# Performance work log

Measured on AMD Instinct MI355X. Metric: run time of the kernel, lower is better.

## Reference

```python
import jax, jax.numpy as jnp
import numpy as np

B, T, H, I, O = 256, 8192, 16, 1, 1


def setup_inputs() -> dict:
    key = jax.random.key(0)
    ks = jax.random.split(key, 8)
    s = 1.0 / np.sqrt(H)  # PyTorch default init scale
    x = jax.random.normal(ks[0], (B, T, I), dtype=jnp.float32)
    h0 = jax.random.normal(ks[1], (1, B, H), dtype=jnp.float32)
    W_ih = jax.random.uniform(ks[2], (H, I), jnp.float32, -s, s)
    W_hh = jax.random.uniform(ks[3], (H, H), jnp.float32, -s, s)
    b_ih = jax.random.uniform(ks[4], (H,), jnp.float32, -s, s)
    b_hh = jax.random.uniform(ks[5], (H,), jnp.float32, -s, s)
    W_out = jax.random.uniform(ks[6], (O, H), jnp.float32, -s, s)
    b_out = jax.random.uniform(ks[7], (O,), jnp.float32, -s, s)
    return {"x": x, "h0": h0, "W_ih": W_ih, "W_hh": W_hh,
            "b_ih": b_ih, "b_hh": b_hh, "W_out": W_out, "b_out": b_out}


def reference(x, h0, W_ih, W_hh, b_ih, b_hh, W_out, b_out):
    # Precompute input projection for all timesteps: [T, B, H]
    xp = jnp.einsum('bti,hi->tbh', x, W_ih) + b_ih + b_hh

    def step(h, xt):
        h_new = jnp.tanh(xt + h @ W_hh.T)  # [B, H]
        return h_new, h_new

    hT, outs = jax.lax.scan(step, h0[0], xp)  # hT: [B,H], outs: [T,B,H]
    out_flat = outs.transpose(1, 0, 2).reshape(-1, H)  # [B*T, H]
    out = (out_flat @ W_out.T + b_out)[None]  # [1, B*T, O]
    return out, hT[None]  # hidden: [1, B, H]
```

## Files before the change

### kernel.cpp

```cpp
#include <hip/hip_runtime.h>

#define ROTI(v, CTRL) __builtin_amdgcn_update_dpp(0, (v), (CTRL), 0xF, 0xF, true)

constexpr int T_LEN  = 8192;
constexpr int BATCH  = 256;
constexpr int HID    = 16;
constexpr int RING   = 128;
constexpr int SLOT_W = 68;
constexpr int CHUNK  = 32;

#define MATVEC(a0_, a1_, a2_, a3_, h_)                                                  \
  asm("s_nop 1\n\t"                                                                     \
      "v_fmac_f32 %[a0], %[h], %[w0]\n\t"                                               \
      "v_mul_f32_dpp %[a1], %[h], %[w4] row_ror:4 row_mask:0xf bank_mask:0xf\n\t"       \
      "v_mul_f32_dpp %[a2], %[h], %[w8] row_ror:8 row_mask:0xf bank_mask:0xf\n\t"       \
      "v_mul_f32_dpp %[a3], %[h], %[w12] row_ror:12 row_mask:0xf bank_mask:0xf\n\t"     \
      "v_fmac_f32_dpp %[a0], %[h], %[w1] row_ror:1 row_mask:0xf bank_mask:0xf\n\t"      \
      "v_fmac_f32_dpp %[a1], %[h], %[w5] row_ror:5 row_mask:0xf bank_mask:0xf\n\t"      \
      "v_fmac_f32_dpp %[a2], %[h], %[w9] row_ror:9 row_mask:0xf bank_mask:0xf\n\t"      \
      "v_fmac_f32_dpp %[a3], %[h], %[w13] row_ror:13 row_mask:0xf bank_mask:0xf\n\t"    \
      "v_fmac_f32_dpp %[a0], %[h], %[w2] row_ror:2 row_mask:0xf bank_mask:0xf\n\t"      \
      "v_fmac_f32_dpp %[a1], %[h], %[w6] row_ror:6 row_mask:0xf bank_mask:0xf\n\t"      \
      "v_fmac_f32_dpp %[a2], %[h], %[w10] row_ror:10 row_mask:0xf bank_mask:0xf\n\t"    \
      "v_fmac_f32_dpp %[a3], %[h], %[w14] row_ror:14 row_mask:0xf bank_mask:0xf\n\t"    \
      "v_fmac_f32_dpp %[a0], %[h], %[w3] row_ror:3 row_mask:0xf bank_mask:0xf\n\t"      \
      "v_fmac_f32_dpp %[a1], %[h], %[w7] row_ror:7 row_mask:0xf bank_mask:0xf\n\t"      \
      "v_fmac_f32_dpp %[a2], %[h], %[w11] row_ror:11 row_mask:0xf bank_mask:0xf\n\t"    \
      "v_fmac_f32_dpp %[a3], %[h], %[w15] row_ror:15 row_mask:0xf bank_mask:0xf\n\t"    \
      : [a0]"+v"(a0_), [a1]"=&v"(a1_), [a2]"=&v"(a2_), [a3]"=&v"(a3_)                  \
      : [h]"v"(h_),                                                                     \
        [w0]"v"(wr0),  [w1]"v"(wr1),  [w2]"v"(wr2),  [w3]"v"(wr3),                      \
        [w4]"v"(wr4),  [w5]"v"(wr5),  [w6]"v"(wr6),  [w7]"v"(wr7),                      \
        [w8]"v"(wr8),  [w9]"v"(wr9),  [w10]"v"(wr10), [w11]"v"(wr11),                   \
        [w12]"v"(wr12), [w13]"v"(wr13), [w14]"v"(wr14), [w15]"v"(wr15))

#define STEP(XV) do {                                                                   \
    float a0 = fmaf((XV), wihK, biasK), a1, a2, a3;                                     \
    MATVEC(a0, a1, a2, a3, h);                                                          \
    float s = (a0 + a1) + (a2 + a3);                                                    \
    float e = __builtin_amdgcn_exp2f(s);                                                \
    h = fmaf(-2.0f, __builtin_amdgcn_rcpf(e + 1.0f), 1.0f);                             \
    *rp = h; rp += SLOT_W;                                                              \
} while (0)

#define BLOCK16(C0, C1, C2, C3) do {                                                    \
    STEP(C0.x); STEP(C0.y); STEP(C0.z); STEP(C0.w);                                     \
    STEP(C1.x); STEP(C1.y); STEP(C1.z); STEP(C1.w);                                     \
    STEP(C2.x); STEP(C2.y); STEP(C2.z); STEP(C2.w);                                     \
    STEP(C3.x); STEP(C3.y); STEP(C3.z); STEP(C3.w);                                     \
} while (0)

__global__ void __launch_bounds__(128, 1)
rnn_fused(const float* __restrict__ x,
          const float* __restrict__ hinit,
          const float* __restrict__ Wih,
          const float* __restrict__ Whh,
          const float* __restrict__ bih,
          const float* __restrict__ bhh,
          const float* __restrict__ Wout,
          const float* __restrict__ boutp,
          float* __restrict__ out)
{
    __shared__ float ring[RING * SLOT_W];
    __shared__ int   syncc[2];
    volatile int* prodc = &syncc[0];
    volatile int* consc = &syncc[1];

    const int tid = (int)threadIdx.x;
    if (tid == 0) { syncc[0] = 0; syncc[1] = 0; }
    __syncthreads();

    if (tid < 64) {
        const int j = tid & 15;
        const int g = tid >> 4;
        const int b = (int)blockIdx.x * 4 + g;

        const int pr  = ROTI(j, 0x121);
        const int dir = (__builtin_amdgcn_readfirstlane(pr) == 1) ? 1 : -1;

        const float K2 = 2.8853900817779268f;
        float wr0  = K2 * Whh[j * HID + ((j + dir * 0)  & 15)];
        float wr1  = K2 * Whh[j * HID + ((j + dir * 1)  & 15)];
        float wr2  = K2 * Whh[j * HID + ((j + dir * 2)  & 15)];
        float wr3  = K2 * Whh[j * HID + ((j + dir * 3)  & 15)];
        float wr4  = K2 * Whh[j * HID + ((j + dir * 4)  & 15)];
        float wr5  = K2 * Whh[j * HID + ((j + dir * 5)  & 15)];
        float wr6  = K2 * Whh[j * HID + ((j + dir * 6)  & 15)];
        float wr7  = K2 * Whh[j * HID + ((j + dir * 7)  & 15)];
        float wr8  = K2 * Whh[j * HID + ((j + dir * 8)  & 15)];
        float wr9  = K2 * Whh[j * HID + ((j + dir * 9)  & 15)];
        float wr10 = K2 * Whh[j * HID + ((j + dir * 10) & 15)];
        float wr11 = K2 * Whh[j * HID + ((j + dir * 11) & 15)];
        float wr12 = K2 * Whh[j * HID + ((j + dir * 12) & 15)];
        float wr13 = K2 * Whh[j * HID + ((j + dir * 13) & 15)];
        float wr14 = K2 * Whh[j * HID + ((j + dir * 14) & 15)];
        float wr15 = K2 * Whh[j * HID + ((j + dir * 15) & 15)];

        const float wihK  = K2 * Wih[j];
        const float biasK = K2 * (bih[j] + bhh[j]);

        float h = hinit[b * HID + j];
        const float* xb = x + (size_t)b * T_LEN;

        float4 c0 = ((const float4*)xb)[0], c1 = ((const float4*)xb)[1],
               c2 = ((const float4*)xb)[2], c3 = ((const float4*)xb)[3];

        for (int t0 = 0; t0 < T_LEN; t0 += 16) {
            if ((t0 & (CHUNK - 1)) == 0) {
                const int need = t0 + CHUNK - RING;
                if (need > 0) {
                    while (*consc < need) { }
                    __asm__ volatile("" ::: "memory");
                }
            }
            const int tn = (t0 + 16) & (T_LEN - 1);
            const float* q = xb + tn;
            float4 n0 = ((const float4*)q)[0], n1 = ((const float4*)q)[1],
                   n2 = ((const float4*)q)[2], n3 = ((const float4*)q)[3];

            float* rp = &ring[(t0 & (RING - 1)) * SLOT_W + g * 17 + j];
            BLOCK16(c0, c1, c2, c3);
            c0 = n0; c1 = n1; c2 = n2; c3 = n3;

            if (((t0 + 16) & (CHUNK - 1)) == 0) {
                __asm__ volatile("s_waitcnt lgkmcnt(0)" ::: "memory");
                *prodc = t0 + 16;
            }
        }

        out[(size_t)BATCH * T_LEN + (size_t)b * HID + j] = h;
    } else {
        const int lane = tid - 64;
        const int tt   = lane & 15;
        const int bs   = lane >> 4;
        const int bg   = (int)blockIdx.x * 4 + bs;

        const float w0  = Wout[0],  w1  = Wout[1],  w2  = Wout[2],  w3  = Wout[3];
        const float w4  = Wout[4],  w5  = Wout[5],  w6  = Wout[6],  w7  = Wout[7];
        const float w8  = Wout[8],  w9  = Wout[9],  w10 = Wout[10], w11 = Wout[11];
        const float w12 = Wout[12], w13 = Wout[13], w14 = Wout[14], w15 = Wout[15];
        const float bo  = boutp[0];

        float* ob = out + (size_t)bg * T_LEN;

        for (int t0 = 0; t0 < T_LEN; t0 += 16) {
            while (*prodc < t0 + 16) { }
            __asm__ volatile("" ::: "memory");

            const float* hr = &ring[((t0 + tt) & (RING - 1)) * SLOT_W + bs * 17];
            float o = bo;
            o = fmaf(hr[0],  w0,  o);
            o = fmaf(hr[1],  w1,  o);
            o = fmaf(hr[2],  w2,  o);
            o = fmaf(hr[3],  w3,  o);
            o = fmaf(hr[4],  w4,  o);
            o = fmaf(hr[5],  w5,  o);
            o = fmaf(hr[6],  w6,  o);
            o = fmaf(hr[7],  w7,  o);
            o = fmaf(hr[8],  w8,  o);
            o = fmaf(hr[9],  w9,  o);
            o = fmaf(hr[10], w10, o);
            o = fmaf(hr[11], w11, o);
            o = fmaf(hr[12], w12, o);
            o = fmaf(hr[13], w13, o);
            o = fmaf(hr[14], w14, o);
            o = fmaf(hr[15], w15, o);
            ob[t0 + tt] = o;

            *consc = t0 + 16;
        }
    }
}

extern "C" void kernel_launch(void* const* d_in, const int* in_sizes, int n_in,
                              void* d_out, int out_size, void* d_ws, size_t ws_size,
                              hipStream_t stream)
{
    const float* x    = (const float*)d_in[0];
    const float* h0   = (const float*)d_in[1];
    const float* Wih  = (const float*)d_in[2];
    const float* Whh  = (const float*)d_in[3];
    const float* bih  = (const float*)d_in[4];
    const float* bhh  = (const float*)d_in[5];
    const float* Wout = (const float*)d_in[6];
    const float* bout = (const float*)d_in[7];
    float* out = (float*)d_out;

    rnn_fused<<<dim3(BATCH / 4), dim3(128), 0, stream>>>(
        x, h0, Wih, Whh, bih, bhh, Wout, bout, out);
}
```

Measured before the change: 541.7 us.

## Interleave two batch recurrences per wavefront and halve the grid

Each producer wavefront now advances two independent batch chains (A and B) together. A single inline-asm block interleaves their DPP matvec with two accumulators each, followed by the exp/rcp tanh, so one chain's instruction latency can be hidden behind the other's. The grid drops from 64 to 32 blocks. The shared ring changes to 64 slots of width 129, and the producer/consumer handshake now happens every 16 steps instead of every 32. The trade-off: each wave issues roughly twice as many instructions per timestep, while the number of sequential timesteps is unchanged.

After: 993.0 us. 83.3% more time.

```diff
diff --git a/kernel.cpp b/kernel.cpp
--- a/kernel.cpp
+++ b/kernel.cpp
@@ -5,49 +5,67 @@
 constexpr int T_LEN  = 8192;
 constexpr int BATCH  = 256;
 constexpr int HID    = 16;
-constexpr int RING   = 128;
-constexpr int SLOT_W = 68;
-constexpr int CHUNK  = 32;
-
-#define MATVEC(a0_, a1_, a2_, a3_, h_)                                                  \
-  asm("s_nop 1\n\t"                                                                     \
-      "v_fmac_f32 %[a0], %[h], %[w0]\n\t"                                               \
-      "v_mul_f32_dpp %[a1], %[h], %[w4] row_ror:4 row_mask:0xf bank_mask:0xf\n\t"       \
-      "v_mul_f32_dpp %[a2], %[h], %[w8] row_ror:8 row_mask:0xf bank_mask:0xf\n\t"       \
-      "v_mul_f32_dpp %[a3], %[h], %[w12] row_ror:12 row_mask:0xf bank_mask:0xf\n\t"     \
-      "v_fmac_f32_dpp %[a0], %[h], %[w1] row_ror:1 row_mask:0xf bank_mask:0xf\n\t"      \
-      "v_fmac_f32_dpp %[a1], %[h], %[w5] row_ror:5 row_mask:0xf bank_mask:0xf\n\t"      \
-      "v_fmac_f32_dpp %[a2], %[h], %[w9] row_ror:9 row_mask:0xf bank_mask:0xf\n\t"      \
-      "v_fmac_f32_dpp %[a3], %[h], %[w13] row_ror:13 row_mask:0xf bank_mask:0xf\n\t"    \
-      "v_fmac_f32_dpp %[a0], %[h], %[w2] row_ror:2 row_mask:0xf bank_mask:0xf\n\t"      \
-      "v_fmac_f32_dpp %[a1], %[h], %[w6] row_ror:6 row_mask:0xf bank_mask:0xf\n\t"      \
-      "v_fmac_f32_dpp %[a2], %[h], %[w10] row_ror:10 row_mask:0xf bank_mask:0xf\n\t"    \
-      "v_fmac_f32_dpp %[a3], %[h], %[w14] row_ror:14 row_mask:0xf bank_mask:0xf\n\t"    \
-      "v_fmac_f32_dpp %[a0], %[h], %[w3] row_ror:3 row_mask:0xf bank_mask:0xf\n\t"      \
-      "v_fmac_f32_dpp %[a1], %[h], %[w7] row_ror:7 row_mask:0xf bank_mask:0xf\n\t"      \
-      "v_fmac_f32_dpp %[a2], %[h], %[w11] row_ror:11 row_mask:0xf bank_mask:0xf\n\t"    \
-      "v_fmac_f32_dpp %[a3], %[h], %[w15] row_ror:15 row_mask:0xf bank_mask:0xf\n\t"    \
-      : [a0]"+v"(a0_), [a1]"=&v"(a1_), [a2]"=&v"(a2_), [a3]"=&v"(a3_)                  \
-      : [h]"v"(h_),                                                                     \
-        [w0]"v"(wr0),  [w1]"v"(wr1),  [w2]"v"(wr2),  [w3]"v"(wr3),                      \
-        [w4]"v"(wr4),  [w5]"v"(wr5),  [w6]"v"(wr6),  [w7]"v"(wr7),                      \
-        [w8]"v"(wr8),  [w9]"v"(wr9),  [w10]"v"(wr10), [w11]"v"(wr11),                   \
+constexpr int RING   = 64;
+constexpr int SLOT_W = 129;
+
+#define STEP2(aA0_, aB0_, hA_, hB_)                                                    \
+  asm("s_nop 1\n\t"                                                                    \
+      "v_fmac_f32 %[aA0], %[hA], %[w0]\n\t"                                            \
+      "v_fmac_f32 %[aB0], %[hB], %[w0]\n\t"                                            \
+      "v_mul_f32_dpp %[aA1], %[hA], %[w1] row_ror:1 row_mask:0xf bank_mask:0xf\n\t"    \
+      "v_mul_f32_dpp %[aB1], %[hB], %[w1] row_ror:1 row_mask:0xf bank_mask:0xf\n\t"    \
+      "v_fmac_f32_dpp %[aA0], %[hA], %[w2] row_ror:2 row_mask:0xf bank_mask:0xf\n\t"   \
+      "v_fmac_f32_dpp %[aB0], %[hB], %[w2] row_ror:2 row_mask:0xf bank_mask:0xf\n\t"   \
+      "v_fmac_f32_dpp %[aA1], %[hA], %[w3] row_ror:3 row_mask:0xf bank_mask:0xf\n\t"   \
+      "v_fmac_f32_dpp %[aB1], %[hB], %[w3] row_ror:3 row_mask:0xf bank_mask:0xf\n\t"   \
+      "v_fmac_f32_dpp %[aA0], %[hA], %[w4] row_ror:4 row_mask:0xf bank_mask:0xf\n\t"   \
+      "v_fmac_f32_dpp %[aB0], %[hB], %[w4] row_ror:4 row_mask:0xf bank_mask:0xf\n\t"   \
+      "v_fmac_f32_dpp %[aA1], %[hA], %[w5] row_ror:5 row_mask:0xf bank_mask:0xf\n\t"   \
+      "v_fmac_f32_dpp %[aB1], %[hB], %[w5] row_ror:5 row_mask:0xf bank_mask:0xf\n\t"   \
+      "v_fmac_f32_dpp %[aA0], %[hA], %[w6] row_ror:6 row_mask:0xf bank_mask:0xf\n\t"   \
+      "v_fmac_f32_dpp %[aB0], %[hB], %[w6] row_ror:6 row_mask:0xf bank_mask:0xf\n\t"   \
+      "v_fmac_f32_dpp %[aA1], %[hA], %[w7] row_ror:7 row_mask:0xf bank_mask:0xf\n\t"   \
+      "v_fmac_f32_dpp %[aB1], %[hB], %[w7] row_ror:7 row_mask:0xf bank_mask:0xf\n\t"   \
+      "v_fmac_f32_dpp %[aA0], %[hA], %[w8] row_ror:8 row_mask:0xf bank_mask:0xf\n\t"   \
+      "v_fmac_f32_dpp %[aB0], %[hB], %[w8] row_ror:8 row_mask:0xf bank_mask:0xf\n\t"   \
+      "v_fmac_f32_dpp %[aA1], %[hA], %[w9] row_ror:9 row_mask:0xf bank_mask:0xf\n\t"   \
+      "v_fmac_f32_dpp %[aB1], %[hB], %[w9] row_ror:9 row_mask:0xf bank_mask:0xf\n\t"   \
+      "v_fmac_f32_dpp %[aA0], %[hA], %[w10] row_ror:10 row_mask:0xf bank_mask:0xf\n\t" \
+      "v_fmac_f32_dpp %[aB0], %[hB], %[w10] row_ror:10 row_mask:0xf bank_mask:0xf\n\t" \
+      "v_fmac_f32_dpp %[aA1], %[hA], %[w11] row_ror:11 row_mask:0xf bank_mask:0xf\n\t" \
+      "v_fmac_f32_dpp %[aB1], %[hB], %[w11] row_ror:11 row_mask:0xf bank_mask:0xf\n\t" \
+      "v_fmac_f32_dpp %[aA0], %[hA], %[w12] row_ror:12 row_mask:0xf bank_mask:0xf\n\t" \
+      "v_fmac_f32_dpp %[aB0], %[hB], %[w12] row_ror:12 row_mask:0xf bank_mask:0xf\n\t" \
+      "v_fmac_f32_dpp %[aA1], %[hA], %[w13] row_ror:13 row_mask:0xf bank_mask:0xf\n\t" \
+      "v_fmac_f32_dpp %[aB1], %[hB], %[w13] row_ror:13 row_mask:0xf bank_mask:0xf\n\t" \
+      "v_fmac_f32_dpp %[aA0], %[hA], %[w14] row_ror:14 row_mask:0xf bank_mask:0xf\n\t" \
+      "v_fmac_f32_dpp %[aB0], %[hB], %[w14] row_ror:14 row_mask:0xf bank_mask:0xf\n\t" \
+      "v_fmac_f32_dpp %[aA1], %[hA], %[w15] row_ror:15 row_mask:0xf bank_mask:0xf\n\t" \
+      "v_fmac_f32_dpp %[aB1], %[hB], %[w15] row_ror:15 row_mask:0xf bank_mask:0xf\n\t" \
+      "v_add_f32 %[aA0], %[aA0], %[aA1]\n\t"                                           \
+      "v_add_f32 %[aB0], %[aB0], %[aB1]\n\t"                                           \
+      "v_exp_f32 %[aA1], %[aA0]\n\t"                                                   \
+      "v_exp_f32 %[aB1], %[aB0]\n\t"                                                   \
+      "v_add_f32 %[aA0], 1.0, %[aA1]\n\t"                                              \
+      "v_add_f32 %[aB0], 1.0, %[aB1]\n\t"                                              \
+      "v_rcp_f32 %[aA1], %[aA0]\n\t"                                                   \
+      "v_rcp_f32 %[aB1], %[aB0]\n\t"                                                   \
+      "v_fma_f32 %[hA], -2.0, %[aA1], 1.0\n\t"                                         \
+      "v_fma_f32 %[hB], -2.0, %[aB1], 1.0\n\t"                                         \
+      : [aA0]"+v"(aA0_), [aB0]"+v"(aB0_),                                              \
+        [aA1]"=&v"(tmpA), [aB1]"=&v"(tmpB),                                            \
+        [hA]"+v"(hA_), [hB]"+v"(hB_)                                                   \
+      : [w0]"v"(wr0),  [w1]"v"(wr1),  [w2]"v"(wr2),  [w3]"v"(wr3),                     \
+        [w4]"v"(wr4),  [w5]"v"(wr5),  [w6]"v"(wr6),  [w7]"v"(wr7),                     \
+        [w8]"v"(wr8),  [w9]"v"(wr9),  [w10]"v"(wr10), [w11]"v"(wr11),                  \
         [w12]"v"(wr12), [w13]"v"(wr13), [w14]"v"(wr14), [w15]"v"(wr15))
 
-#define STEP(XV) do {                                                                   \
-    float a0 = fmaf((XV), wihK, biasK), a1, a2, a3;                                     \
-    MATVEC(a0, a1, a2, a3, h);                                                          \
-    float s = (a0 + a1) + (a2 + a3);                                                    \
-    float e = __builtin_amdgcn_exp2f(s);                                                \
-    h = fmaf(-2.0f, __builtin_amdgcn_rcpf(e + 1.0f), 1.0f);                             \
-    *rp = h; rp += SLOT_W;                                                              \
-} while (0)
-
-#define BLOCK16(C0, C1, C2, C3) do {                                                    \
-    STEP(C0.x); STEP(C0.y); STEP(C0.z); STEP(C0.w);                                     \
-    STEP(C1.x); STEP(C1.y); STEP(C1.z); STEP(C1.w);                                     \
-    STEP(C2.x); STEP(C2.y); STEP(C2.z); STEP(C2.w);                                     \
-    STEP(C3.x); STEP(C3.y); STEP(C3.z); STEP(C3.w);                                     \
+#define POSITION(XA, XB, POS) do {                                                     \
+    float aA0 = fmaf((XA), wihK, biasK);                                               \
+    float aB0 = fmaf((XB), wihK, biasK);                                               \
+    STEP2(aA0, aB0, hA, hB);                                                           \
+    rp[(POS) * SLOT_W]      = hA;                                                      \
+    rp[(POS) * SLOT_W + 64] = hB;                                                      \
 } while (0)
 
 __global__ void __launch_bounds__(128, 1)
@@ -73,7 +91,8 @@
     if (tid < 64) {
         const int j = tid & 15;
         const int g = tid >> 4;
-        const int b = (int)blockIdx.x * 4 + g;
+        const int bA = (int)blockIdx.x * 8 + g;
+        const int bB = bA + 4;
 
         const int pr  = ROTI(j, 0x121);
         const int dir = (__builtin_amdgcn_readfirstlane(pr) == 1) ? 1 : -1;
@@ -99,41 +118,66 @@
         const float wihK  = K2 * Wih[j];
         const float biasK = K2 * (bih[j] + bhh[j]);
 
-        float h = hinit[b * HID + j];
-        const float* xb = x + (size_t)b * T_LEN;
-
-        float4 c0 = ((const float4*)xb)[0], c1 = ((const float4*)xb)[1],
-               c2 = ((const float4*)xb)[2], c3 = ((const float4*)xb)[3];
+        float hA = hinit[bA * HID + j];
+        float hB = hinit[bB * HID + j];
+        float tmpA, tmpB;
+
+        const float* xbA = x + (size_t)bA * T_LEN;
+        const float* xbB = x + (size_t)bB * T_LEN;
+
+        float4 qA0 = ((const float4*)xbA)[0], qA1 = ((const float4*)xbA)[1],
+               qA2 = ((const float4*)xbA)[2], qA3 = ((const float4*)xbA)[3];
+        float4 qB0 = ((const float4*)xbB)[0], qB1 = ((const float4*)xbB)[1],
+               qB2 = ((const float4*)xbB)[2], qB3 = ((const float4*)xbB)[3];
 
         for (int t0 = 0; t0 < T_LEN; t0 += 16) {
-            if ((t0 & (CHUNK - 1)) == 0) {
-                const int need = t0 + CHUNK - RING;
-                if (need > 0) {
-                    while (*consc < need) { }
-                    __asm__ volatile("" ::: "memory");
-                }
+            const int need = t0 + 16 - RING;
+            if (need > 0) {
+                while (*consc < need) { }
+                __asm__ volatile("" ::: "memory");
             }
             const int tn = (t0 + 16) & (T_LEN - 1);
-            const float* q = xb + tn;
-            float4 n0 = ((const float4*)q)[0], n1 = ((const float4*)q)[1],
-                   n2 = ((const float4*)q)[2], n3 = ((const float4*)q)[3];
-
-            float* rp = &ring[(t0 & (RING - 1)) * SLOT_W + g * 17 + j];
-            BLOCK16(c0, c1, c2, c3);
-            c0 = n0; c1 = n1; c2 = n2; c3 = n3;
-
-            if (((t0 + 16) & (CHUNK - 1)) == 0) {
-                __asm__ volatile("s_waitcnt lgkmcnt(0)" ::: "memory");
-                *prodc = t0 + 16;
-            }
+            const float* qa = xbA + tn;
+            const float* qb = xbB + tn;
+            float4 nA0 = ((const float4*)qa)[0], nA1 = ((const float4*)qa)[1],
+                   nA2 = ((const float4*)qa)[2], nA3 = ((const float4*)qa)[3];
+            float4 nB0 = ((const float4*)qb)[0], nB1 = ((const float4*)qb)[1],
+                   nB2 = ((const float4*)qb)[2], nB3 = ((const float4*)qb)[3];
+
+            float* rp = &ring[(t0 & (RING - 1)) * SLOT_W + g * 16 + j];
+
+            POSITION(qA0.x, qB0.x, 0);
+            POSITION(qA0.y, qB0.y, 1);
+            POSITION(qA0.z, qB0.z, 2);
+            POSITION(qA0.w, qB0.w, 3);
+            POSITION(qA1.x, qB1.x, 4);
+            POSITION(qA1.y, qB1.y, 5);
+            POSITION(qA1.z, qB1.z, 6);
+            POSITION(qA1.w, qB1.w, 7);
+            POSITION(qA2.x, qB2.x, 8);
+            POSITION(qA2.y, qB2.y, 9);
+            POSITION(qA2.z, qB2.z, 10);
+            POSITION(qA2.w, qB2.w, 11);
+            POSITION(qA3.x, qB3.x, 12);
+            POSITION(qA3.y, qB3.y, 13);
+            POSITION(qA3.z, qB3.z, 14);
+            POSITION(qA3.w, qB3.w, 15);
+
+            qA0 = nA0; qA1 = nA1; qA2 = nA2; qA3 = nA3;
+            qB0 = nB0; qB1 = nB1; qB2 = nB2; qB3 = nB3;
+
+            __asm__ volatile("s_waitcnt lgkmcnt(0)" ::: "memory");
+            *prodc = t0 + 16;
         }
 
-        out[(size_t)BATCH * T_LEN + (size_t)b * HID + j] = h;
+        out[(size_t)BATCH * T_LEN + (size_t)bA * HID + j] = hA;
+        out[(size_t)BATCH * T_LEN + (size_t)bB * HID + j] = hB;
     } else {
         const int lane = tid - 64;
         const int tt   = lane & 15;
         const int bs   = lane >> 4;
-        const int bg   = (int)blockIdx.x * 4 + bs;
+        const int bgA  = (int)blockIdx.x * 8 + bs;
+        const int bgB  = bgA + 4;
 
         const float w0  = Wout[0],  w1  = Wout[1],  w2  = Wout[2],  w3  = Wout[3];
         const float w4  = Wout[4],  w5  = Wout[5],  w6  = Wout[6],  w7  = Wout[7];
@@ -141,31 +185,40 @@
         const float w12 = Wout[12], w13 = Wout[13], w14 = Wout[14], w15 = Wout[15];
         const float bo  = boutp[0];
 
-        float* ob = out + (size_t)bg * T_LEN;
+        float* obA = out + (size_t)bgA * T_LEN;
+        float* obB = out + (size_t)bgB * T_LEN;
 
         for (int t0 = 0; t0 < T_LEN; t0 += 16) {
             while (*prodc < t0 + 16) { }
             __asm__ volatile("" ::: "memory");
 
-            const float* hr = &ring[((t0 + tt) & (RING - 1)) * SLOT_W + bs * 17];
-            float o = bo;
-            o = fmaf(hr[0],  w0,  o);
-            o = fmaf(hr[1],  w1,  o);
-            o = fmaf(hr[2],  w2,  o);
-            o = fmaf(hr[3],  w3,  o);
-            o = fmaf(hr[4],  w4,  o);
-            o = fmaf(hr[5],  w5,  o);
-            o = fmaf(hr[6],  w6,  o);
-            o = fmaf(hr[7],  w7,  o);
-            o = fmaf(hr[8],  w8,  o);
-            o = fmaf(hr[9],  w9,  o);
-            o = fmaf(hr[10], w10, o);
-            o = fmaf(hr[11], w11, o);
-            o = fmaf(hr[12], w12, o);
-            o = fmaf(hr[13], w13, o);
-            o = fmaf(hr[14], w14, o);
-            o = fmaf(hr[15], w15, o);
-            ob[t0 + tt] = o;
+            const float* base = &ring[((t0 + tt) & (RING - 1)) * SLOT_W + bs * 16];
+            {
+                const float* hr = base;
+                float o = bo;
+                o = fmaf(hr[0],  w0,  o); o = fmaf(hr[1],  w1,  o);
+                o = fmaf(hr[2],  w2,  o); o = fmaf(hr[3],  w3,  o);
+                o = fmaf(hr[4],  w4,  o); o = fmaf(hr[5],  w5,  o);
+                o = fmaf(hr[6],  w6,  o); o = fmaf(hr[7],  w7,  o);
+                o = fmaf(hr[8],  w8,  o); o = fmaf(hr[9],  w9,  o);
+                o = fmaf(hr[10], w10, o); o = fmaf(hr[11], w11, o);
+                o = fmaf(hr[12], w12, o); o = fmaf(hr[13], w13, o);
+                o = fmaf(hr[14], w14, o); o = fmaf(hr[15], w15, o);
+                obA[t0 + tt] = o;
+            }
+            {
+                const float* hr = base + 64;
+                float o = bo;
+                o = fmaf(hr[0],  w0,  o); o = fmaf(hr[1],  w1,  o);
+                o = fmaf(hr[2],  w2,  o); o = fmaf(hr[3],  w3,  o);
+                o = fmaf(hr[4],  w4,  o); o = fmaf(hr[5],  w5,  o);
+                o = fmaf(hr[6],  w6,  o); o = fmaf(hr[7],  w7,  o);
+                o = fmaf(hr[8],  w8,  o); o = fmaf(hr[9],  w9,  o);
+                o = fmaf(hr[10], w10, o); o = fmaf(hr[11], w11, o);
+                o = fmaf(hr[12], w12, o); o = fmaf(hr[13], w13, o);
+                o = fmaf(hr[14], w14, o); o = fmaf(hr[15], w15, o);
+                obB[t0 + tt] = o;
+            }
 
             *consc = t0 + 16;
         }
@@ -186,6 +239,6 @@
     const float* bout = (const float*)d_in[7];
     float* out = (float*)d_out;
 
-    rnn_fused<<<dim3(BATCH / 4), dim3(128), 0, stream>>>(
+    rnn_fused<<<dim3(BATCH / 8), dim3(128), 0, stream>>>(
         x, h0, Wih, Whh, bih, bhh, Wout, bout, out);
 }
```

## Use packed fp16 dot products for recurrence and output projection

Applied to the files above, without the earlier changes.

Packs the hidden state and recurrent weights into fp16 pairs, using v_dot2 with DPP-shuffled operands to halve the multiply-add count per step. The rcp instruction is replaced with a bit-trick initial guess plus two Newton steps. The ring buffer stores packed halves, shrinks, and is synchronized every 16 steps. This trades accuracy (fp16 hidden state and weights across a long recurrence) and extra DPP and convert latency on the serial chain for fewer FMAs.

New measurement: 592.3 us. 9.3% more time.

```diff
diff --git a/kernel.cpp b/kernel.cpp
--- a/kernel.cpp
+++ b/kernel.cpp
@@ -1,53 +1,44 @@
 #include <hip/hip_runtime.h>
 
-#define ROTI(v, CTRL) __builtin_amdgcn_update_dpp(0, (v), (CTRL), 0xF, 0xF, true)
+typedef decltype(__builtin_amdgcn_cvt_pkrtz(0.0f, 0.0f)) h2;
+
+#define DPPI(v, CTRL) __builtin_amdgcn_update_dpp(0, (v), (CTRL), 0xF, 0xF, true)
+#define H2(x)  __builtin_bit_cast(h2, (x))
+#define I32(x) __builtin_bit_cast(int, (x))
 
 constexpr int T_LEN  = 8192;
 constexpr int BATCH  = 256;
 constexpr int HID    = 16;
-constexpr int RING   = 128;
-constexpr int SLOT_W = 68;
-constexpr int CHUNK  = 32;
+constexpr int RING   = 64;
+constexpr int SLOT_W = 67;
 
-#define MATVEC(a0_, a1_, a2_, a3_, h_)                                                  \
-  asm("s_nop 1\n\t"                                                                     \
-      "v_fmac_f32 %[a0], %[h], %[w0]\n\t"                                               \
-      "v_mul_f32_dpp %[a1], %[h], %[w4] row_ror:4 row_mask:0xf bank_mask:0xf\n\t"       \
-      "v_mul_f32_dpp %[a2], %[h], %[w8] row_ror:8 row_mask:0xf bank_mask:0xf\n\t"       \
-      "v_mul_f32_dpp %[a3], %[h], %[w12] row_ror:12 row_mask:0xf bank_mask:0xf\n\t"     \
-      "v_fmac_f32_dpp %[a0], %[h], %[w1] row_ror:1 row_mask:0xf bank_mask:0xf\n\t"      \
-      "v_fmac_f32_dpp %[a1], %[h], %[w5] row_ror:5 row_mask:0xf bank_mask:0xf\n\t"      \
-      "v_fmac_f32_dpp %[a2], %[h], %[w9] row_ror:9 row_mask:0xf bank_mask:0xf\n\t"      \
-      "v_fmac_f32_dpp %[a3], %[h], %[w13] row_ror:13 row_mask:0xf bank_mask:0xf\n\t"    \
-      "v_fmac_f32_dpp %[a0], %[h], %[w2] row_ror:2 row_mask:0xf bank_mask:0xf\n\t"      \
-      "v_fmac_f32_dpp %[a1], %[h], %[w6] row_ror:6 row_mask:0xf bank_mask:0xf\n\t"      \
-      "v_fmac_f32_dpp %[a2], %[h], %[w10] row_ror:10 row_mask:0xf bank_mask:0xf\n\t"    \
-      "v_fmac_f32_dpp %[a3], %[h], %[w14] row_ror:14 row_mask:0xf bank_mask:0xf\n\t"    \
-      "v_fmac_f32_dpp %[a0], %[h], %[w3] row_ror:3 row_mask:0xf bank_mask:0xf\n\t"      \
-      "v_fmac_f32_dpp %[a1], %[h], %[w7] row_ror:7 row_mask:0xf bank_mask:0xf\n\t"      \
-      "v_fmac_f32_dpp %[a2], %[h], %[w11] row_ror:11 row_mask:0xf bank_mask:0xf\n\t"    \
-      "v_fmac_f32_dpp %[a3], %[h], %[w15] row_ror:15 row_mask:0xf bank_mask:0xf\n\t"    \
-      : [a0]"+v"(a0_), [a1]"=&v"(a1_), [a2]"=&v"(a2_), [a3]"=&v"(a3_)                  \
-      : [h]"v"(h_),                                                                     \
-        [w0]"v"(wr0),  [w1]"v"(wr1),  [w2]"v"(wr2),  [w3]"v"(wr3),                      \
-        [w4]"v"(wr4),  [w5]"v"(wr5),  [w6]"v"(wr6),  [w7]"v"(wr7),                      \
-        [w8]"v"(wr8),  [w9]"v"(wr9),  [w10]"v"(wr10), [w11]"v"(wr11),                   \
-        [w12]"v"(wr12), [w13]"v"(wr13), [w14]"v"(wr14), [w15]"v"(wr15))
+__device__ __forceinline__ float rcp_nr(float d) {
+    float r = __int_as_float(0x7EF311C3 - __float_as_int(d));
+    r = r * fmaf(-d, r, 2.0f);
+    r = r * fmaf(-d, r, 2.0f);
+    return r;
+}
 
-#define STEP(XV) do {                                                                   \
-    float a0 = fmaf((XV), wihK, biasK), a1, a2, a3;                                     \
-    MATVEC(a0, a1, a2, a3, h);                                                          \
-    float s = (a0 + a1) + (a2 + a3);                                                    \
-    float e = __builtin_amdgcn_exp2f(s);                                                \
-    h = fmaf(-2.0f, __builtin_amdgcn_rcpf(e + 1.0f), 1.0f);                             \
-    *rp = h; rp += SLOT_W;                                                              \
-} while (0)
-
-#define BLOCK16(C0, C1, C2, C3) do {                                                    \
-    STEP(C0.x); STEP(C0.y); STEP(C0.z); STEP(C0.w);                                     \
-    STEP(C1.x); STEP(C1.y); STEP(C1.z); STEP(C1.w);                                     \
-    STEP(C2.x); STEP(C2.y); STEP(C2.z); STEP(C2.w);                                     \
-    STEP(C3.x); STEP(C3.y); STEP(C3.z); STEP(C3.w);                                     \
+#define STEP(XV, KOFF) do {                                                   \
+    int q1 = DPPI(Pi, 0x122), q2 = DPPI(Pi, 0x124), q3 = DPPI(Pi, 0x126);     \
+    int q4 = DPPI(Pi, 0x128), q5 = DPPI(Pi, 0x12A), q6 = DPPI(Pi, 0x12C);     \
+    int q7 = DPPI(Pi, 0x12E);                                                 \
+    float a0 = fmaf((XV), wihK, biasK);                                       \
+    a0 = __builtin_amdgcn_fdot2(H2(Pi), w0, a0, false);                       \
+    a0 = __builtin_amdgcn_fdot2(H2(q1), w1, a0, false);                       \
+    a0 = __builtin_amdgcn_fdot2(H2(q2), w2, a0, false);                       \
+    a0 = __builtin_amdgcn_fdot2(H2(q3), w3, a0, false);                       \
+    float a1 = __builtin_amdgcn_fdot2(H2(q4), w4, 0.0f, false);               \
+    a1 = __builtin_amdgcn_fdot2(H2(q5), w5, a1, false);                       \
+    a1 = __builtin_amdgcn_fdot2(H2(q6), w6, a1, false);                       \
+    a1 = __builtin_amdgcn_fdot2(H2(q7), w7, a1, false);                       \
+    float e  = __builtin_amdgcn_exp2f(a0 + a1);                               \
+    float dd = e + 1.0f;                                                      \
+    float r  = rcp_nr(dd);                                                    \
+    h = fmaf(-2.0f, r, 1.0f);                                                 \
+    int hn = DPPI(__float_as_int(h), 0x121);                                  \
+    Pi = I32(__builtin_amdgcn_cvt_pkrtz(h, __int_as_float(hn)));              \
+    rbase[(KOFF) * SLOT_W] = Pi;                                              \
 } while (0)
 
 __global__ void __launch_bounds__(128, 1)
@@ -61,8 +52,8 @@
           const float* __restrict__ boutp,
           float* __restrict__ out)
 {
-    __shared__ float ring[RING * SLOT_W];
-    __shared__ int   syncc[2];
+    __shared__ int ring[RING * SLOT_W];
+    __shared__ int syncc[2];
     volatile int* prodc = &syncc[0];
     volatile int* consc = &syncc[1];
 
@@ -75,57 +66,56 @@
         const int g = tid >> 4;
         const int b = (int)blockIdx.x * 4 + g;
 
-        const int pr  = ROTI(j, 0x121);
+        const int pr  = DPPI(j, 0x121);
         const int dir = (__builtin_amdgcn_readfirstlane(pr) == 1) ? 1 : -1;
 
         const float K2 = 2.8853900817779268f;
-        float wr0  = K2 * Whh[j * HID + ((j + dir * 0)  & 15)];
-        float wr1  = K2 * Whh[j * HID + ((j + dir * 1)  & 15)];
-        float wr2  = K2 * Whh[j * HID + ((j + dir * 2)  & 15)];
-        float wr3  = K2 * Whh[j * HID + ((j + dir * 3)  & 15)];
-        float wr4  = K2 * Whh[j * HID + ((j + dir * 4)  & 15)];
-        float wr5  = K2 * Whh[j * HID + ((j + dir * 5)  & 15)];
-        float wr6  = K2 * Whh[j * HID + ((j + dir * 6)  & 15)];
-        float wr7  = K2 * Whh[j * HID + ((j + dir * 7)  & 15)];
-        float wr8  = K2 * Whh[j * HID + ((j + dir * 8)  & 15)];
-        float wr9  = K2 * Whh[j * HID + ((j + dir * 9)  & 15)];
-        float wr10 = K2 * Whh[j * HID + ((j + dir * 10) & 15)];
-        float wr11 = K2 * Whh[j * HID + ((j + dir * 11) & 15)];
-        float wr12 = K2 * Whh[j * HID + ((j + dir * 12) & 15)];
-        float wr13 = K2 * Whh[j * HID + ((j + dir * 13) & 15)];
-        float wr14 = K2 * Whh[j * HID + ((j + dir * 14) & 15)];
-        float wr15 = K2 * Whh[j * HID + ((j + dir * 15) & 15)];
+
+        h2 w0, w1, w2, w3, w4, w5, w6, w7;
+        {
+#define PACKW(Q, DST) do {                                                    \
+            float lo = K2 * Whh[j * HID + ((j + dir * (2 * (Q)))     & 15)];  \
+            float hi = K2 * Whh[j * HID + ((j + dir * (2 * (Q) + 1)) & 15)];  \
+            DST = __builtin_amdgcn_cvt_pkrtz(lo, hi);                         \
+        } while (0)
+            PACKW(0, w0); PACKW(1, w1); PACKW(2, w2); PACKW(3, w3);
+            PACKW(4, w4); PACKW(5, w5); PACKW(6, w6); PACKW(7, w7);
+#undef PACKW
+        }
 
         const float wihK  = K2 * Wih[j];
         const float biasK = K2 * (bih[j] + bhh[j]);
 
         float h = hinit[b * HID + j];
+        int hn0 = DPPI(__float_as_int(h), 0x121);
+        int Pi  = I32(__builtin_amdgcn_cvt_pkrtz(h, __int_as_float(hn0)));
+
         const float* xb = x + (size_t)b * T_LEN;
-
         float4 c0 = ((const float4*)xb)[0], c1 = ((const float4*)xb)[1],
                c2 = ((const float4*)xb)[2], c3 = ((const float4*)xb)[3];
 
         for (int t0 = 0; t0 < T_LEN; t0 += 16) {
-            if ((t0 & (CHUNK - 1)) == 0) {
-                const int need = t0 + CHUNK - RING;
-                if (need > 0) {
-                    while (*consc < need) { }
-                    __asm__ volatile("" ::: "memory");
-                }
+            const int need = t0 + 16 - RING;
+            if (need > 0) {
+                while (*consc < need) { }
+                __asm__ volatile("" ::: "memory");
             }
             const int tn = (t0 + 16) & (T_LEN - 1);
             const float* q = xb + tn;
             float4 n0 = ((const float4*)q)[0], n1 = ((const float4*)q)[1],
                    n2 = ((const float4*)q)[2], n3 = ((const float4*)q)[3];
 
-            float* rp = &ring[(t0 & (RING - 1)) * SLOT_W + g * 17 + j];
-            BLOCK16(c0, c1, c2, c3);
+            int* rbase = &ring[(t0 & (RING - 1)) * SLOT_W + g * 16 + j];
+
+            STEP(c0.x, 0);  STEP(c0.y, 1);  STEP(c0.z, 2);  STEP(c0.w, 3);
+            STEP(c1.x, 4);  STEP(c1.y, 5);  STEP(c1.z, 6);  STEP(c1.w, 7);
+            STEP(c2.x, 8);  STEP(c2.y, 9);  STEP(c2.z, 10); STEP(c2.w, 11);
+            STEP(c3.x, 12); STEP(c3.y, 13); STEP(c3.z, 14); STEP(c3.w, 15);
+
             c0 = n0; c1 = n1; c2 = n2; c3 = n3;
 
-            if (((t0 + 16) & (CHUNK - 1)) == 0) {
-                __asm__ volatile("s_waitcnt lgkmcnt(0)" ::: "memory");
-                *prodc = t0 + 16;
-            }
+            __asm__ volatile("s_waitcnt lgkmcnt(0)" ::: "memory");
+            *prodc = t0 + 16;
         }
 
         out[(size_t)BATCH * T_LEN + (size_t)b * HID + j] = h;
@@ -135,11 +125,19 @@
         const int bs   = lane >> 4;
         const int bg   = (int)blockIdx.x * 4 + bs;
 
-        const float w0  = Wout[0],  w1  = Wout[1],  w2  = Wout[2],  w3  = Wout[3];
-        const float w4  = Wout[4],  w5  = Wout[5],  w6  = Wout[6],  w7  = Wout[7];
-        const float w8  = Wout[8],  w9  = Wout[9],  w10 = Wout[10], w11 = Wout[11];
-        const float w12 = Wout[12], w13 = Wout[13], w14 = Wout[14], w15 = Wout[15];
-        const float bo  = boutp[0];
+        const int pr  = DPPI(lane & 15, 0x121);
+        const int dir = (__builtin_amdgcn_readfirstlane(pr) == 1) ? 1 : -1;
+
+        h2 u0, u1, u2, u3, u4, u5, u6, u7;
+#define PACKU(Q, DST) do {                                                    \
+        float lo = Wout[2 * (Q)];                                             \
+        float hi = Wout[(2 * (Q) + dir) & 15];                                \
+        DST = __builtin_amdgcn_cvt_pkrtz(lo, hi);                             \
+    } while (0)
+        PACKU(0, u0); PACKU(1, u1); PACKU(2, u2); PACKU(3, u3);
+        PACKU(4, u4); PACKU(5, u5); PACKU(6, u6); PACKU(7, u7);
+#undef PACKU
+        const float bo = boutp[0];
 
         float* ob = out + (size_t)bg * T_LEN;
 
@@ -147,27 +145,19 @@
             while (*prodc < t0 + 16) { }
             __asm__ volatile("" ::: "memory");
 
-            const float* hr = &ring[((t0 + tt) & (RING - 1)) * SLOT_W + bs * 17];
+            const int* rr = &ring[((t0 + tt) & (RING - 1)) * SLOT_W + bs * 16];
             float o = bo;
-            o = fmaf(hr[0],  w0,  o);
-            o = fmaf(hr[1],  w1,  o);
-            o = fmaf(hr[2],  w2,  o);
-            o = fmaf(hr[3],  w3,  o);
-            o = fmaf(hr[4],  w4,  o);
-            o = fmaf(hr[5],  w5,  o);
-            o = fmaf(hr[6],  w6,  o);
-            o = fmaf(hr[7],  w7,  o);
-            o = fmaf(hr[8],  w8,  o);
-            o = fmaf(hr[9],  w9,  o);
-            o = fmaf(hr[10], w10, o);
-            o = fmaf(hr[11], w11, o);
-            o = fmaf(hr[12], w12, o);
-            o = fmaf(hr[13], w13, o);
-            o = fmaf(hr[14], w14, o);
-            o = fmaf(hr[15], w15, o);
+            o = __builtin_amdgcn_fdot2(H2(rr[0]),  u0, o, false);
+            o = __builtin_amdgcn_fdot2(H2(rr[2]),  u1, o, false);
+            o = __builtin_amdgcn_fdot2(H2(rr[4]),  u2, o, false);
+            o = __builtin_amdgcn_fdot2(H2(rr[6]),  u3, o, false);
+            o = __builtin_amdgcn_fdot2(H2(rr[8]),  u4, o, false);
+            o = __builtin_amdgcn_fdot2(H2(rr[10]), u5, o, false);
+            o = __builtin_amdgcn_fdot2(H2(rr[12]), u6, o, false);
+            o = __builtin_amdgcn_fdot2(H2(rr[14]), u7, o, false);
             ob[t0 + tt] = o;
 
-            *consc = t0 + 16;
+            if (lane == 0) *consc = t0 + 16;
         }
     }
 }
```
